# Performance work log

Hardware: AMD Instinct MI355X
Metric: run time of the kernel (lower is better)

The kernel has to match this reference:

```python
import jax, jax.numpy as jnp
import numpy as np

# ---- constants from init_kwargs (mode='local', channel='G') ----
MEAN = 127.5
STD = 50.0
BINS = np.array([-2.4, -1.6, -0.8, 0.0, 0.8, 1.6, 2.4])
NB = len(BINS) + 1            # 8 quantization levels
DIST = [1, 2, 3]
THETA = [0.0, np.pi / 4, np.pi / 2, 3 * np.pi / 4]
MASK = 17
STRIDE = 4
BIN_EDGES = 0.5 + BINS / 6.0
# skimage greycomatrix offsets: (round(sin(t)*d), round(cos(t)*d)), ordered d-major
OFFSETS = [(int(np.round(np.sin(t) * d)), int(np.round(np.cos(t) * d)))
           for d in DIST for t in THETA]


def setup_inputs() -> dict:
    key = jax.random.key(0)
    x = jax.random.uniform(key, (8, 3, 256, 256), dtype=jnp.float32) * 255.0
    return {"x": x}


def _features(x):
    img = x[:, 1, :, :]                       # channel 'G'
    img = jnp.where(img < 10.0, 0.0, img)     # imgs[imgs < 10] = 0
    B, H, W = img.shape
    N = (H - MASK) // STRIDE + 1              # 60 windows per axis

    # sliding windows -> (B, N, N, MASK, MASK)
    r = (jnp.arange(N) * STRIDE)[:, None] + jnp.arange(MASK)[None, :]
    win = img[:, r[:, None, :, None], r[None, :, None, :]]
    Nw = B * N * N
    flat = win.reshape(Nw, MASK * MASK)

    # ---- stat over nonzero pixels (numpy population std) ----
    mask = flat != 0.0
    n_safe = jnp.maximum(mask.sum(-1), 1).astype(flat.dtype)
    mean = jnp.where(mask, flat, 0.0).sum(-1) / n_safe
    std = jnp.sqrt((jnp.where(mask, flat - mean[:, None], 0.0) ** 2).sum(-1) / n_safe)
    mx = jnp.where(mask, flat, -jnp.inf).max(-1)
    mn = jnp.where(mask, flat, jnp.inf).min(-1)
    stat = jnp.stack([mean, std, (mx - mean) / (std + 1e-9), (mean - mn) / (std + 1e-9)], -1)

    # ---- quantize ----
    q = jnp.digitize(((flat - MEAN) / STD + 3.0) / 6.0, jnp.asarray(BIN_EDGES, flat.dtype))

    # ---- histogram (density over ALL pixels, drop first & last bin) ----
    onehot = (q[..., None] == jnp.arange(NB)).astype(flat.dtype)
    hist_feat = onehot.sum(1)[:, 1:NB - 1] / flat.shape[1]   # (Nw, len(BINS)-1)

    # ---- GLCM per (dist, theta) offset, symmetric + normed ----
    qm = q.reshape(Nw, MASK, MASK)
    rows = jnp.arange(Nw)[:, None]
    glcms = []
    for dr, dc in OFFSETS:
        if dc >= 0:
            i = qm[:, :MASK - dr, :MASK - dc]
            j = qm[:, dr:, dc:]
        else:
            i = qm[:, :MASK - dr, -dc:]
            j = qm[:, dr:, :MASK + dc]
        pair = (i * NB + j).reshape(Nw, -1)
        cnt = jnp.zeros((Nw, NB * NB), flat.dtype).at[rows, pair].add(1.0)
        P = cnt.reshape(Nw, NB, NB)
        P = P + P.transpose(0, 2, 1)                               # symmetric
        P = P / jnp.maximum(P.sum((1, 2), keepdims=True), 1e-12)   # normed
        glcms.append(P)
    G = jnp.stack(glcms, 1)          # (Nw, 12, NB, NB)
    g = G[:, :, 1:, 1:]              # crop level 0 (zeros)
    L = NB - 1

    # greycoprops renormalizes the (cropped) GLCM internally
    Pn = g / jnp.maximum(g.sum((2, 3), keepdims=True), 1e-12)
    I = jnp.arange(L, dtype=flat.dtype)
    diff2 = (I[:, None] - I[None, :]) ** 2
    contrast = (Pn * diff2).sum((2, 3))
    homog = (Pn / (1.0 + diff2)).sum((2, 3))
    energy = jnp.sqrt((Pn ** 2).sum((2, 3)))
    Pi = Pn.sum(3)
    Pj = Pn.sum(2)
    mui = (Pi * I).sum(-1)
    muj = (Pj * I).sum(-1)
    sdi = jnp.sqrt((Pi * (I - mui[..., None]) ** 2).sum(-1))
    sdj = jnp.sqrt((Pj * (I - muj[..., None]) ** 2).sum(-1))
    cov = (Pn * (I[:, None] - mui[..., None, None]) * (I[None, :] - muj[..., None, None])).sum((2, 3))
    corr = jnp.where(sdi * sdj < 1e-15, 1.0, cov / jnp.maximum(sdi * sdj, 1e-15))
    entropy = -(g * jnp.log2(g + 1e-8)).sum((2, 3))   # on cropped, non-renormed g

    glcm_feat = jnp.concatenate([contrast, homog, energy, corr, entropy], -1)  # (Nw, 60)
    feats = jnp.concatenate([stat, hist_feat, glcm_feat], -1)                  # (Nw, 70)

    # windows with max == 0 yield all-zero feature vectors
    feats = jnp.where((flat.max(-1) == 0.0)[:, None], 0.0, feats)

    Fdim = feats.shape[-1]
    feats = feats.reshape(B, N, N, Fdim)
    total = feats.sum((1, 2))
    nz = (feats != 0).sum((1, 2)).astype(flat.dtype)
    return total / (nz + 1e-9)            # (B, 70)


def reference(x):
    return _features(x)
```

## Files before the change

kernel.cpp:

```cpp
#include <hip/hip_runtime.h>
#include <cmath>

#define NPIX   289
#define NU     10
#define NF     70
#define NFP    80
#define NWX    60
#define IMG_W  256
#define IMG_HW 65536
#define NWIN   28800
#define ACC    560
#define ACCP   640
#define WPB    2
#define WPW    4
#define NBLK   (NWIN / (WPB * WPW))
#define GLS    29

__device__ __constant__ int c_s2u[12] = {0,1,2,3,4,1,5,3,6,7,8,9};

constexpr int JOFF[NU] = {1, 18, 17, 16, 2, 34, 3, 36, 51, 32};
constexpr float INV2N[NU] = {1.f/544.f, 1.f/512.f, 1.f/544.f, 1.f/512.f, 1.f/510.f,
                             1.f/510.f, 1.f/476.f, 1.f/450.f, 1.f/476.f, 1.f/450.f};

struct CMs { unsigned m[10]; };
constexpr CMs mkcm(int dc) {
    CMs c{};
    for (int t = 0; t < NPIX; ++t) {
        int col = t % 17;
        bool ok = (dc > 0) ? (col >= dc) : (col <= 16 + dc);
        if (ok) c.m[t >> 5] |= 1u << (t & 31);
    }
    return c;
}
constexpr CMs CMp1 = mkcm(1), CMp2 = mkcm(2), CMp3 = mkcm(3);
constexpr CMs CMn1 = mkcm(-1), CMn2 = mkcm(-2);

struct alignas(32) FtE { float w, d2, inv, si, sii, sij, q0, q1; };
struct FtTab { FtE e[28]; };
constexpr FtTab mkft() {
    FtTab t{};
    int n = 0;
    for (int a = 1; a <= 7; ++a)
        for (int b = a; b <= 7; ++b) {
            int i = a - 1, j = b - 1;
            float w  = (a == b) ? 1.f : 2.f;
            float d2 = (float)((i - j) * (i - j));
            t.e[n] = FtE{w, d2, 1.f / (1.f + d2),
                         0.5f * (float)(i + j),
                         0.5f * (float)(i * i + j * j),
                         (float)(i * j), 0.f, 0.f};
            ++n;
        }
    return t;
}
__device__ __constant__ FtTab c_ft = mkft();

template<int O>
__device__ __forceinline__ int gcnt(const unsigned* __restrict__ M,
                                    const unsigned* __restrict__ ma) {
    constexpr int wq = JOFF[O] >> 5;
    constexpr int rr = JOFF[O] & 31;
    constexpr int nw = (288 - JOFF[O]) / 32 + 1;
    int acc = 0;
#pragma unroll
    for (int w = 0; w < nw; ++w) {
        unsigned sh = (rr == 0) ? M[w + wq]
                                : __builtin_amdgcn_alignbit(M[w + wq + 1], M[w + wq], rr);
        acc += __popc(ma[w] & sh);
    }
    return acc;
}

#define DPP_F(oldv, srcv, ctrl, rm) \
    __int_as_float(__builtin_amdgcn_update_dpp((oldv), __float_as_int(srcv), (ctrl), (rm), 0xF, false))

__device__ __forceinline__ float dpp_wsum(float v) {
    v += DPP_F(0, v, 0x111, 0xF);
    v += DPP_F(0, v, 0x112, 0xF);
    v += DPP_F(0, v, 0x114, 0xF);
    v += DPP_F(0, v, 0x118, 0xF);
    v += DPP_F(0, v, 0x142, 0xA);
    v += DPP_F(0, v, 0x143, 0xC);
    return __int_as_float(__builtin_amdgcn_readlane(__float_as_int(v), 63));
}
__device__ __forceinline__ float dpp_wmax(float v) {
    v = fmaxf(v, DPP_F(__float_as_int(v), v, 0x111, 0xF));
    v = fmaxf(v, DPP_F(__float_as_int(v), v, 0x112, 0xF));
    v = fmaxf(v, DPP_F(__float_as_int(v), v, 0x114, 0xF));
    v = fmaxf(v, DPP_F(__float_as_int(v), v, 0x118, 0xF));
    v = fmaxf(v, DPP_F(__float_as_int(v), v, 0x142, 0xA));
    v = fmaxf(v, DPP_F(__float_as_int(v), v, 0x143, 0xC));
    return __int_as_float(__builtin_amdgcn_readlane(__float_as_int(v), 63));
}
__device__ __forceinline__ float dpp_wmin(float v) {
    v = fminf(v, DPP_F(__float_as_int(v), v, 0x111, 0xF));
    v = fminf(v, DPP_F(__float_as_int(v), v, 0x112, 0xF));
    v = fminf(v, DPP_F(__float_as_int(v), v, 0x114, 0xF));
    v = fminf(v, DPP_F(__float_as_int(v), v, 0x118, 0xF));
    v = fminf(v, DPP_F(__float_as_int(v), v, 0x142, 0xA));
    v = fminf(v, DPP_F(__float_as_int(v), v, 0x143, 0xC));
    return __int_as_float(__builtin_amdgcn_readlane(__float_as_int(v), 63));
}

__device__ __forceinline__ float bperm_f(int addr, float v) {
    return __int_as_float(__builtin_amdgcn_ds_bpermute(addr, __float_as_int(v)));
}

__global__ __launch_bounds__(128, 8) void feat_kernel(const float* __restrict__ x,
                                                      float* __restrict__ ptot,
                                                      float* __restrict__ pnz,
                                                      int setmask) {
    __shared__ float s_g[WPB][NU * GLS];
    __shared__ float s_uf[WPB][5][NU];
    __shared__ float s_s10[WPB][10];

    const int lane = threadIdx.x & 63;
    const int wid  = threadIdx.x >> 6;
    const int b     = blockIdx.x & 7;
    const int lbid  = blockIdx.x >> 3;
    const int rem0  = lbid * (WPB * WPW) + wid * WPW;
    const int wy    = rem0 / NWX;
    const int wx0   = rem0 - wy * NWX;
    const int widx0 = b * 3600 + rem0;
    const float* img0 = x + (size_t)(b * 3 + 1) * IMG_HW + (wy * 4) * IMG_W + wx0 * 4;

    float* gl  = s_g[wid];
    float (*uf)[NU] = s_uf[wid];
    float* s10 = s_s10[wid];

    const int l49 = (lane < 49) ? lane : 48;
    const int ba  = l49 / 7 + 1;
    const int bb  = l49 - (ba - 1) * 7 + 1;
    const int partner = (bb - 1) * 7 + (ba - 1);
    const int paddr   = partner << 2;
    const unsigned long long xm0a = (ba & 1) ? 0ull : ~0ull;
    const unsigned long long xm1a = (ba & 2) ? 0ull : ~0ull;
    const unsigned long long xm2a = (ba & 4) ? 0ull : ~0ull;
    const int amin  = min(ba, bb);
    const int idx28 = 8 * (amin - 1) - ((amin * (amin - 1)) >> 1) + (max(ba, bb) - amin);
    const bool wr   = (lane < 49) && (ba <= bb);
    const int fo  = lane & 15;
    const int sub = lane >> 4;
    const int xa16 = (lane ^ 16) << 2;
    const int xa32 = (lane ^ 32) << 2;
    const int obase = b * NFP;

    int off[5];
#pragma unroll
    for (int k = 0; k < 5; ++k) {
        int t = lane + k * 64;
        int r = t / 17;
        off[k] = r * (IMG_W - 17) + t;
    }
    const bool v4 = (lane < NPIX - 256);

    auto PROC = [&](const float (&pv)[5], int widx) {
        float lsum = 0.f, lss = 0.f, lmax = -1e30f, lmin = 1e30f;
        int n = 0, c1 = 0, c2 = 0, c3 = 0, c4 = 0, c5 = 0, c6 = 0;
        unsigned ma32[10];
#pragma unroll
        for (int k = 0; k < 5; ++k) {
            float p = pv[k];
            float val = (p < 10.f) ? 0.f : p;
            if (k == 4) val = v4 ? val : 0.f;
            int qq = (int)fmaf(val, 0.025f, 0.8125f);
            lsum += val;
            float d = (val != 0.f) ? (val - 127.5f) : 0.f;
            lss = fmaf(d, d, lss);
            lmax = fmaxf(lmax, val);
            lmin = fminf(lmin, (val != 0.f) ? val : 1e30f);
            unsigned long long p0 = __ballot(qq & 1);
            unsigned long long p1 = __ballot(qq & 2);
            unsigned long long p2 = __ballot(qq & 4);
            n  += __popcll(p0 | p1 | p2);
            c1 += __popcll(p0 & ~p1 & ~p2);
            c2 += __popcll(~p0 & p1 & ~p2);
            c3 += __popcll(p0 & p1 & ~p2);
            c4 += __popcll(~p0 & ~p1 & p2);
            c5 += __popcll(p0 & ~p1 & p2);
            c6 += __popcll(~p0 & p1 & p2);
            unsigned long long mA = (p0 ^ xm0a) & (p1 ^ xm1a) & (p2 ^ xm2a);
            ma32[2*k]   = (unsigned)mA;
            ma32[2*k+1] = (unsigned)(mA >> 32);
        }

        if (n == 0) return;

        unsigned mv0[10];
#pragma unroll
        for (int w = 0; w < 10; ++w)
            mv0[w] = (unsigned)__builtin_amdgcn_ds_bpermute(paddr, (int)ma32[w]);

        const float fn   = (float)n;
        const float sum  = dpp_wsum(lsum);
        const float ss   = dpp_wsum(lss);
        const float mx   = dpp_wmax(lmax);
        const float mn   = dpp_wmin(lmin);
        const float mean = sum / fn;
        const float mc   = mean - 127.5f;
        const float var  = fmaxf(ss / fn - mc * mc, 0.f);
        const float stdv = sqrtf(var);

        if (lane == 0) {
            s10[0] = mean;
            s10[1] = stdv;
            s10[2] = (mx - mean) / (stdv + 1e-9f);
            s10[3] = (mean - mn) / (stdv + 1e-9f);
            s10[4] = (float)c1 * (1.f / 289.f);
            s10[5] = (float)c2 * (1.f / 289.f);
            s10[6] = (float)c3 * (1.f / 289.f);
            s10[7] = (float)c4 * (1.f / 289.f);
            s10[8] = (float)c5 * (1.f / 289.f);
            s10[9] = (float)c6 * (1.f / 289.f);
        }

        int cnta[NU];
        {
            cnta[2] = gcnt<2>(mv0, ma32);
            cnta[5] = gcnt<5>(mv0, ma32);
            cnta[8] = gcnt<8>(mv0, ma32);
            unsigned mv[10];
#pragma unroll
            for (int w = 0; w < 10; ++w) mv[w] = mv0[w] & CMp1.m[w];
            cnta[0] = gcnt<0>(mv, ma32);
            cnta[1] = gcnt<1>(mv, ma32);
#pragma unroll
            for (int w = 0; w < 10; ++w) mv[w] = mv0[w] & CMp2.m[w];
            cnta[4] = gcnt<4>(mv, ma32);
            cnta[7] = gcnt<7>(mv, ma32);
#pragma unroll
            for (int w = 0; w < 10; ++w) mv[w] = mv0[w] & CMp3.m[w];
            cnta[6] = gcnt<6>(mv, ma32);
#pragma unroll
            for (int w = 0; w < 10; ++w) mv[w] = mv0[w] & CMn1.m[w];
            cnta[3] = gcnt<3>(mv, ma32);
#pragma unroll
            for (int w = 0; w < 10; ++w) mv[w] = mv0[w] & CMn2.m[w];
            cnta[9] = gcnt<9>(mv, ma32);
        }

#pragma unroll
        for (int o = 0; o < NU; ++o) {
            int pc = __builtin_amdgcn_ds_bpermute(paddr, cnta[o]);
            float g = (float)(cnta[o] + pc) * INV2N[o];
            if (wr) gl[o * GLS + idx28] = g;
        }

        float gsum=0.f, entU=0.f, conU=0.f, homU=0.f, g2=0.f, siU=0.f, siiU=0.f, sijU=0.f;
        if (fo < NU) {
#pragma unroll
            for (int i = 0; i < 7; ++i) {
                const int e = sub + 4 * i;
                FtE c = c_ft.e[e];
                float g  = gl[fo * GLS + e];
                float gw = g * c.w;
                float l  = __log2f(g + 1e-8f);
                gsum += gw;
                entU  = fmaf(gw, l,      entU);
                conU  = fmaf(gw, c.d2,   conU);
                homU  = fmaf(gw, c.inv,  homU);
                g2    = fmaf(gw, g,      g2);
                siU   = fmaf(gw, c.si,   siU);
                siiU  = fmaf(gw, c.sii,  siiU);
                sijU  = fmaf(gw, c.sij,  sijU);
            }
        }
        gsum += bperm_f(xa16, gsum);  entU += bperm_f(xa16, entU);
        conU += bperm_f(xa16, conU);  homU += bperm_f(xa16, homU);
        g2   += bperm_f(xa16, g2);    siU  += bperm_f(xa16, siU);
        siiU += bperm_f(xa16, siiU);  sijU += bperm_f(xa16, sijU);
        gsum += bperm_f(xa32, gsum);  entU += bperm_f(xa32, entU);
        conU += bperm_f(xa32, conU);  homU += bperm_f(xa32, homU);
        g2   += bperm_f(xa32, g2);    siU  += bperm_f(xa32, siU);
        siiU += bperm_f(xa32, siiU);  sijU += bperm_f(xa32, sijU);

        if (fo < NU && sub == 0) {
            const float invg = 1.f / fmaxf(gsum, 1e-12f);
            const float si  = siU  * invg;
            const float sii = siiU * invg;
            const float sij = sijU * invg;
            const float varg = fmaxf(sii - si * si, 0.f);
            const float cov  = sij - si * si;
            uf[0][fo] = conU * invg;
            uf[1][fo] = homU * invg;
            uf[2][fo] = sqrtf(g2) * invg;
            uf[3][fo] = (varg < 1e-15f) ? 1.f : cov / fmaxf(varg, 1e-15f);
            uf[4][fo] = -entU;
        }

        const int setbase = (widx & setmask) * ACCP;
        for (int t = lane; t < NF; t += 64) {
            float f;
            if (t < 10) {
                f = s10[t];
            } else {
                int u    = t - 10;
                int grp  = u / 12;
                int slot = u - grp * 12;
                f = uf[grp][c_s2u[slot]];
            }
            atomicAdd(&ptot[setbase + obase + t], f);
            if (t >= 4 && t <= 9 && f != 0.f)
                atomicAdd(&pnz[setbase + obase + t], 1.f);
        }
        if (lane == 0)
            atomicAdd(&pnz[setbase + obase], 1.f);
    };

#define LOADW(buf, iw) { \
        const float* ip = img0 + (iw) * 4; \
        buf[0] = ip[off[0]]; buf[1] = ip[off[1]]; buf[2] = ip[off[2]]; \
        buf[3] = ip[off[3]]; buf[4] = ip[off[4]]; }

    float bufA[5], bufB[5];
    LOADW(bufA, 0)
    LOADW(bufB, 1)
    PROC(bufA, widx0 + 0);
    LOADW(bufA, 2)
    PROC(bufB, widx0 + 1);
    LOADW(bufB, 3)
    PROC(bufA, widx0 + 2);
    PROC(bufB, widx0 + 3);
#undef LOADW
}

__global__ void reduce_kernel(const float* __restrict__ ptot,
                              const float* __restrict__ pnz,
                              float* __restrict__ out, int nset) {
    int t = blockIdx.x * blockDim.x + threadIdx.x;
    if (t >= ACC) return;
    int b = t / NF;
    int u = t - b * NF;
    int pa = b * NFP + u;
    bool hist = (u >= 4 && u <= 9);
    int nzidx = hist ? pa : b * NFP;
    float s = 0.f, nz = 0.f;
    for (int k = 0; k < nset; ++k) {
        s  += ptot[(size_t)k * ACCP + pa];
        nz += pnz[(size_t)k * ACCP + nzidx];
    }
    out[t] = s / (nz + 1e-9f);
}

extern "C" void kernel_launch(void* const* d_in, const int* in_sizes, int n_in,
                              void* d_out, int out_size, void* d_ws, size_t ws_size,
                              hipStream_t stream) {
    (void)in_sizes; (void)n_in; (void)out_size;
    const float* x = (const float*)d_in[0];
    float* out = (float*)d_out;

    const size_t per_set = (size_t)2 * ACCP * sizeof(float);
    int maxs = (ws_size >= per_set) ? (int)(ws_size / per_set) : 1;
    int nset = 1;
    while ((nset * 2) <= maxs && nset < 64) nset <<= 1;

    float* ptot = (float*)d_ws;
    float* pnz  = ptot + (size_t)nset * ACCP;

    hipMemsetAsync(d_ws, 0, (size_t)nset * per_set, stream);
    feat_kernel<<<dim3(NBLK), dim3(WPB * 64), 0, stream>>>(x, ptot, pnz, nset - 1);
    reduce_kernel<<<dim3((ACC + 255) / 256), dim3(256), 0, stream>>>(ptot, pnz, out, nset);
}
```

Baseline: 136.7 us.

## Accumulate per-wave features in registers and flush atomics once per wave

Each wave now sums its windows' feature values in registers through precomputed LDS read pointers and issues one batch of global atomics at the end, where before it issued atomics after every window. Windows per wave drop from four to two, which doubles the block count, and the block-to-window mapping becomes linear. The atomic partial-sum layout drops its padding from 80 to 70 floats per batch. This cuts atomic traffic by half per window, at the cost of less load/compute overlap per wave and a different spread of contention over the partial-sum sets.

```diff
diff --git a/kernel.cpp b/kernel.cpp
--- a/kernel.cpp
+++ b/kernel.cpp
@@ -4,15 +4,13 @@
 #define NPIX   289
 #define NU     10
 #define NF     70
-#define NFP    80
 #define NWX    60
 #define IMG_W  256
 #define IMG_HW 65536
 #define NWIN   28800
 #define ACC    560
-#define ACCP   640
 #define WPB    2
-#define WPW    4
+#define WPW    2
 #define NBLK   (NWIN / (WPB * WPW))
 #define GLS    29
 
@@ -116,12 +114,12 @@
 
     const int lane = threadIdx.x & 63;
     const int wid  = threadIdx.x >> 6;
-    const int b     = blockIdx.x & 7;
-    const int lbid  = blockIdx.x >> 3;
-    const int rem0  = lbid * (WPB * WPW) + wid * WPW;
+    const int gw    = blockIdx.x * WPB + wid;
+    const int widx0 = gw * WPW;
+    const int b     = widx0 / 3600;
+    const int rem0  = widx0 - b * 3600;
     const int wy    = rem0 / NWX;
     const int wx0   = rem0 - wy * NWX;
-    const int widx0 = b * 3600 + rem0;
     const float* img0 = x + (size_t)(b * 3 + 1) * IMG_HW + (wy * 4) * IMG_W + wx0 * 4;
 
     float* gl  = s_g[wid];
@@ -143,7 +141,17 @@
     const int sub = lane >> 4;
     const int xa16 = (lane ^ 16) << 2;
     const int xa32 = (lane ^ 32) << 2;
-    const int obase = b * NFP;
+
+    const float* rb0;
+    if (lane < 10) {
+        rb0 = &s10[lane];
+    } else {
+        int u = lane - 10, g = u / 12;
+        rb0 = &uf[g][c_s2u[u - g * 12]];
+    }
+    const int u1 = (lane < 6) ? (lane + 54) : 54;
+    const int g1 = u1 / 12;
+    const float* rb1 = &uf[g1][c_s2u[u1 - g1 * 12]];
 
     int off[5];
 #pragma unroll
@@ -154,7 +162,9 @@
     }
     const bool v4 = (lane < NPIX - 256);
 
-    auto PROC = [&](const float (&pv)[5], int widx) {
+    float facc0 = 0.f, facc1 = 0.f, nzh = 0.f, wcnt = 0.f;
+
+    auto PROC = [&](const float (&pv)[5]) {
         float lsum = 0.f, lss = 0.f, lmax = -1e30f, lmin = 1e30f;
         int n = 0, c1 = 0, c2 = 0, c3 = 0, c4 = 0, c5 = 0, c6 = 0;
         unsigned ma32[10];
@@ -185,6 +195,7 @@
         }
 
         if (n == 0) return;
+        wcnt += 1.f;
 
         unsigned mv0[10];
 #pragma unroll
@@ -288,40 +299,29 @@
             uf[4][fo] = -entU;
         }
 
-        const int setbase = (widx & setmask) * ACCP;
-        for (int t = lane; t < NF; t += 64) {
-            float f;
-            if (t < 10) {
-                f = s10[t];
-            } else {
-                int u    = t - 10;
-                int grp  = u / 12;
-                int slot = u - grp * 12;
-                f = uf[grp][c_s2u[slot]];
-            }
-            atomicAdd(&ptot[setbase + obase + t], f);
-            if (t >= 4 && t <= 9 && f != 0.f)
-                atomicAdd(&pnz[setbase + obase + t], 1.f);
-        }
-        if (lane == 0)
-            atomicAdd(&pnz[setbase + obase], 1.f);
+        float f0 = *rb0;
+        facc0 += f0;
+        if (lane >= 4 && lane <= 9) nzh += (f0 != 0.f) ? 1.f : 0.f;
+        if (lane < 6) facc1 += *rb1;
     };
 
-#define LOADW(buf, iw) { \
-        const float* ip = img0 + (iw) * 4; \
-        buf[0] = ip[off[0]]; buf[1] = ip[off[1]]; buf[2] = ip[off[2]]; \
-        buf[3] = ip[off[3]]; buf[4] = ip[off[4]]; }
-
     float bufA[5], bufB[5];
-    LOADW(bufA, 0)
-    LOADW(bufB, 1)
-    PROC(bufA, widx0 + 0);
-    LOADW(bufA, 2)
-    PROC(bufB, widx0 + 1);
-    LOADW(bufB, 3)
-    PROC(bufA, widx0 + 2);
-    PROC(bufB, widx0 + 3);
-#undef LOADW
+    {
+        const float* ipA = img0;
+        const float* ipB = img0 + 4;
+        bufA[0] = ipA[off[0]]; bufA[1] = ipA[off[1]]; bufA[2] = ipA[off[2]];
+        bufA[3] = ipA[off[3]]; bufA[4] = ipA[off[4]];
+        bufB[0] = ipB[off[0]]; bufB[1] = ipB[off[1]]; bufB[2] = ipB[off[2]];
+        bufB[3] = ipB[off[3]]; bufB[4] = ipB[off[4]];
+    }
+    PROC(bufA);
+    PROC(bufB);
+
+    const int setbase = (gw & setmask) * ACC + b * NF;
+    atomicAdd(&ptot[setbase + lane], facc0);
+    if (lane < 6) atomicAdd(&ptot[setbase + 64 + lane], facc1);
+    if (lane >= 4 && lane <= 9 && nzh != 0.f) atomicAdd(&pnz[setbase + lane], nzh);
+    if (lane == 0 && wcnt != 0.f) atomicAdd(&pnz[setbase], wcnt);
 }
 
 __global__ void reduce_kernel(const float* __restrict__ ptot,
@@ -331,13 +331,12 @@
     if (t >= ACC) return;
     int b = t / NF;
     int u = t - b * NF;
-    int pa = b * NFP + u;
     bool hist = (u >= 4 && u <= 9);
-    int nzidx = hist ? pa : b * NFP;
+    int nzidx = hist ? t : b * NF;
     float s = 0.f, nz = 0.f;
     for (int k = 0; k < nset; ++k) {
-        s  += ptot[(size_t)k * ACCP + pa];
-        nz += pnz[(size_t)k * ACCP + nzidx];
+        s  += ptot[(size_t)k * ACC + t];
+        nz += pnz[(size_t)k * ACC + nzidx];
     }
     out[t] = s / (nz + 1e-9f);
 }
@@ -349,13 +348,13 @@
     const float* x = (const float*)d_in[0];
     float* out = (float*)d_out;
 
-    const size_t per_set = (size_t)2 * ACCP * sizeof(float);
+    const size_t per_set = (size_t)2 * ACC * sizeof(float);
     int maxs = (ws_size >= per_set) ? (int)(ws_size / per_set) : 1;
     int nset = 1;
     while ((nset * 2) <= maxs && nset < 64) nset <<= 1;
 
     float* ptot = (float*)d_ws;
-    float* pnz  = ptot + (size_t)nset * ACCP;
+    float* pnz  = ptot + (size_t)nset * ACC;
 
     hipMemsetAsync(d_ws, 0, (size_t)nset * per_set, stream);
     feat_kernel<<<dim3(NBLK), dim3(WPB * 64), 0, stream>>>(x, ptot, pnz, nset - 1);
```

New measurement: 119.5 us. 1.14x faster.
